# Kernel optimization log

Hardware: AMD Instinct MI355X
Metric: run time of the kernel (lower is better)

Reference implementation:

```python
import itertools
import jax, jax.numpy as jnp
import numpy as np

B, N, C, H = 4, 48, 16, 64
CIN = [48, 64, 128, 192]   # per-order MLP input dims after expand/reduce/concat/permute
COUT = 16

def _exclude_mask(n, cnt, dtype):
    # mask[i1..icnt] = 1 iff all object indices are pairwise distinct
    if cnt <= 1:
        return jnp.ones((n,), dtype=dtype)
    idx = [jnp.arange(n).reshape((1,) * d + (n,) + (1,) * (cnt - 1 - d)) for d in range(cnt)]
    m = jnp.ones((n,) * cnt, dtype=bool)
    for a in range(cnt):
        for b in range(a + 1, cnt):
            m = m & (idx[a] != idx[b])
    return m.astype(dtype)

def _reduce(x, dim):
    # x: [B] + [n]*dim + [C]; exists=max / forall=min over last object axis, exclude_self mask
    n = x.shape[1]
    m = _exclude_mask(n, dim, x.dtype)[..., None]  # [n]*dim + [1], broadcasts over B and C
    ex = jnp.max(x * m, axis=-2)
    fa = jnp.min(x * m + (1.0 - m), axis=-2)
    out = jnp.stack([ex, fa], axis=-1)  # interleave (exists, forall) per channel
    return out.reshape(out.shape[:-2] + (out.shape[-2] * 2,))

def _expand(x, dim, n):
    # insert a new object axis at position dim+1 and broadcast to n
    return jnp.broadcast_to(jnp.expand_dims(x, dim + 1), x.shape[:dim + 1] + (n,) + x.shape[dim + 1:])

def _permute(x, dim):
    # concat all permutations of the object axes along channels
    if dim <= 1:
        return x
    parts = [jnp.transpose(x, (0,) + p + (dim + 1,)) for p in itertools.permutations(range(1, dim + 1))]
    return jnp.concatenate(parts, axis=-1)

def _logic(x, W1, b1, W2, b2):
    # LogicInferenceLayer: Linear -> ReLU -> Linear -> Sigmoid on channel axis
    return jax.nn.sigmoid(jax.nn.relu(x @ W1 + b1) @ W2 + b2)

def setup_inputs() -> dict:
    key = jax.random.key(0)
    ks = jax.random.split(key, 24)
    inp = {
        'x0': jax.random.uniform(ks[0], (B, C), dtype=jnp.float32),
        'x1': jax.random.uniform(ks[1], (B, N, C), dtype=jnp.float32),
        'x2': jax.random.uniform(ks[2], (B, N, N, C), dtype=jnp.float32),
        'x3': jax.random.uniform(ks[3], (B, N, N, N, C), dtype=jnp.float32),
    }
    for o, cin in enumerate(CIN):
        inp[f'W1_{o}'] = jax.random.normal(ks[4 + 4 * o], (cin, H), dtype=jnp.float32) * 0.05
        inp[f'b1_{o}'] = jnp.zeros((H,), dtype=jnp.float32)
        inp[f'W2_{o}'] = jax.random.normal(ks[5 + 4 * o], (H, COUT), dtype=jnp.float32) * 0.05
        inp[f'b2_{o}'] = jnp.zeros((COUT,), dtype=jnp.float32)
    return inp

def reference(x0, x1, x2, x3,
              W1_0, b1_0, W2_0, b2_0,
              W1_1, b1_1, W2_1, b2_1,
              W1_2, b1_2, W2_2, b2_2,
              W1_3, b1_3, W2_3, b2_3):
    n = x1.shape[1]
    # order 0: [self, reduce(order1)]
    t0 = jnp.concatenate([x0, _reduce(x1, 1)], axis=-1)
    y0 = _logic(t0, W1_0, b1_0, W2_0, b2_0)
    # order 1: [expand(order0), self, reduce(order2)]
    t1 = jnp.concatenate([_expand(x0, 0, n), x1, _reduce(x2, 2)], axis=-1)
    y1 = _logic(t1, W1_1, b1_1, W2_1, b2_1)
    # order 2: [expand(order1), self, reduce(order3)], permute 2 object axes
    t2 = jnp.concatenate([_expand(x1, 1, n), x2, _reduce(x3, 3)], axis=-1)
    y2 = _logic(_permute(t2, 2), W1_2, b1_2, W2_2, b2_2)
    # order 3 (max order): [expand(order2), self], permute 3 object axes
    t3 = jnp.concatenate([_expand(x2, 2, n), x3], axis=-1)
    y3 = _logic(_permute(t3, 3), W1_3, b1_3, W2_3, b2_3)
    return (y0, y1, y2, y3)
```

## Files before the change

kernel.cpp:

```cpp
#include <hip/hip_runtime.h>
#include <hip/hip_bf16.h>


typedef __bf16 bf16x8 __attribute__((ext_vector_type(8)));
typedef unsigned short us8 __attribute__((ext_vector_type(8)));
typedef float f32x4 __attribute__((ext_vector_type(4)));

#define NPAIR 589824
#define NRED3 294912
#define NX3   7077888

__device__ __forceinline__ unsigned short f2bf(float f) {
    __hip_bfloat16 h = __float2bfloat16(f);
    return __builtin_bit_cast(unsigned short, h);
}
__device__ __forceinline__ unsigned int pk2(float a, float b) {
    return (unsigned int)f2bf(a) | ((unsigned int)f2bf(b) << 16);
}
__device__ __forceinline__ float bflo(unsigned int u) {
    return __builtin_bit_cast(float, u << 16);
}
__device__ __forceinline__ float bfhi(unsigned int u) {
    return __builtin_bit_cast(float, u & 0xffff0000u);
}
__device__ __forceinline__ float sigmoidf_(float z) {
    return 1.0f / (1.0f + __expf(-z));
}
__device__ __forceinline__ bf16x8 ld_bf8(const unsigned short* p) {
    return __builtin_bit_cast(bf16x8, *(const us8*)p);
}
__device__ __forceinline__ bf16x8 pack8(float4 a, float4 b) {
    us8 u;
    u[0] = f2bf(a.x); u[1] = f2bf(a.y); u[2] = f2bf(a.z); u[3] = f2bf(a.w);
    u[4] = f2bf(b.x); u[5] = f2bf(b.y); u[6] = f2bf(b.z); u[7] = f2bf(b.w);
    return __builtin_bit_cast(bf16x8, u);
}

__global__ __launch_bounds__(192) void perm3_kernel(
    const float* __restrict__ x3,
    unsigned short* __restrict__ X0, unsigned short* __restrict__ XA,
    unsigned short* __restrict__ XB)
{
    const int g = blockIdx.x;
    const int m2 = g % 48, t1 = g / 48, m1 = t1 % 48, b = t1 / 48;
    const int t = threadIdx.x;
    const int m3 = t >> 2, cq = (t & 3) * 4;
    const float4 v = *(const float4*)(x3 + (size_t)g * 768 + m3 * 16 + cq);
    const uint2 u = make_uint2(pk2(v.x, v.y), pk2(v.z, v.w));
    *(uint2*)(X0 + (size_t)g * 768 + m3 * 16 + cq) = u;
    *(uint2*)(XA + (((size_t)(b * 48 + m1) * 48 + m3) * 48 + m2) * 16 + cq) = u;
    *(uint2*)(XB + (((size_t)(b * 48 + m2) * 48 + m3) * 48 + m1) * 16 + cq) = u;
}

__global__ __launch_bounds__(256) void phaseA_kernel(
    const float* __restrict__ x2, const float* __restrict__ W1,
    const float* __restrict__ b1,
    float* __restrict__ wsA, unsigned short* __restrict__ wsB,
    unsigned short* __restrict__ wsC)
{
    __shared__ float xr[4][32];
    const int t = threadIdx.x;
    if (t < 128) {
        const int pr2 = t >> 5, c = t & 31;
        const int gg = blockIdx.x * 4 + pr2;
        const int bb = gg / 2304, pp2 = gg % 2304, P = pp2 / 48, Q = pp2 % 48;
        const float* base = x2 + (size_t)bb * 36864;
        xr[pr2][c] = (c < 16) ? base[(P * 48 + Q) * 16 + c]
                              : base[(Q * 48 + P) * 16 + (c - 16)];
    }
    __syncthreads();
    const int pr = t >> 6, h = t & 63;
    const int g = blockIdx.x * 4 + pr;
    float a = b1[h], bacc = 0.f, cacc = 0.f;
#pragma unroll
    for (int c = 0; c < 16; ++c) {
        const float xpq = xr[pr][c], xqp = xr[pr][16 + c];
        a    += xpq * W1[(  0 + c) * 64 + h] + xqp * W1[( 64 + c) * 64 + h];
        bacc += xpq * W1[( 32 + c) * 64 + h] + xqp * W1[( 96 + c) * 64 + h];
        cacc += xpq * W1[(128 + c) * 64 + h] + xqp * W1[(160 + c) * 64 + h];
    }
    const size_t o = (size_t)g * 64 + h;
    wsA[o] = a;
    wsB[o] = f2bf(bacc);
    wsC[o] = f2bf(cacc);
}

__global__ __launch_bounds__(192, 3) void y3_kernel(
    const unsigned short* __restrict__ X0,
    const unsigned short* __restrict__ XA,
    const unsigned short* __restrict__ XB,
    const float* __restrict__ W1, const float* __restrict__ W2,
    const float* __restrict__ b2,
    const float* __restrict__ wsA,
    const unsigned short* __restrict__ wsB,
    const unsigned short* __restrict__ wsC,
    float* __restrict__ out)
{
    __shared__ __align__(16) unsigned short w1t[64 * 104];
    const int t = threadIdx.x;
    const int w = t >> 6, lane = t & 63, lr = lane & 15, lg = lane >> 4;

#pragma unroll
    for (int p = 0; p < 16; ++p) {
        const int e = p * 192 + t;
        const int h = e & 63, kk = (e >> 6) * 2;
        const int r0 = 16 + ((kk >> 4) << 5) + (kk & 15);
        *(unsigned int*)(w1t + h * 104 + kk) =
            pk2(W1[r0 * 64 + h], W1[(r0 + 1) * 64 + h]);
    }
    __syncthreads();

    bf16x8 w1f[4][3];
#pragma unroll
    for (int n = 0; n < 4; ++n)
#pragma unroll
        for (int ks = 0; ks < 3; ++ks)
            w1f[n][ks] = ld_bf8(w1t + (16 * n + lr) * 104 + 32 * ks + 8 * lg);

    bf16x8 w2f[2];
#pragma unroll
    for (int m = 0; m < 2; ++m) {
        us8 u;
#pragma unroll
        for (int e = 0; e < 8; ++e) {
            const int ch = 16 * (e >> 1) + 4 * lg + 2 * (e & 1) + m;
            u[e] = f2bf(W2[ch * 16 + lr]);
        }
        w2f[m] = __builtin_bit_cast(bf16x8, u);
    }
    const float4 b2v = *(const float4*)(b2 + 4 * lg);
    const int row = 16 * w + lr;
    const int roff = row * 16 + 8 * (lg & 1);
    const bool hi = (lg >> 1) != 0;

    for (int it = 0; it < 4; ++it) {
        const int g = blockIdx.x * 4 + it;
        const int b = g / 2304, pp = g % 2304, i = pp / 48, j = pp % 48;
        const size_t blkIJ = ((size_t)(b * 48 + i) * 48 + j) * 768;
        const size_t blkJI = ((size_t)(b * 48 + j) * 48 + i) * 768;
        const unsigned short* p0 = (hi ? XA + blkIJ : X0 + blkIJ) + roff;
        const unsigned short* p1 = (hi ? XB + blkIJ : X0 + blkJI) + roff;
        const unsigned short* p2 = (hi ? XB + blkJI : XA + blkJI) + roff;
        const bf16x8 xf0 = ld_bf8(p0);
        const bf16x8 xf1 = ld_bf8(p1);
        const bf16x8 xf2 = ld_bf8(p2);

        f32x4 acc[4];
#pragma unroll
        for (int n = 0; n < 4; ++n) {
            acc[n] = f32x4{0.f, 0.f, 0.f, 0.f};
            acc[n] = __builtin_amdgcn_mfma_f32_16x16x32_bf16(w1f[n][0], xf0, acc[n], 0, 0, 0);
            acc[n] = __builtin_amdgcn_mfma_f32_16x16x32_bf16(w1f[n][1], xf1, acc[n], 0, 0, 0);
            acc[n] = __builtin_amdgcn_mfma_f32_16x16x32_bf16(w1f[n][2], xf2, acc[n], 0, 0, 0);
        }
        const size_t baseB = ((size_t)((b * 48 + i) * 48 + row)) * 64 + 4 * lg;
        const size_t baseC = ((size_t)((b * 48 + j) * 48 + row)) * 64 + 4 * lg;
        const size_t baseA = ((size_t)((b * 48 + i) * 48 + j)) * 64 + 4 * lg;
#pragma unroll
        for (int n = 0; n < 4; ++n) {
            const uint2 Bu = *(const uint2*)(wsB + baseB + 16 * n);
            const uint2 Cu = *(const uint2*)(wsC + baseC + 16 * n);
            const float4 Au = *(const float4*)(wsA + baseA + 16 * n);
            acc[n][0] = fmaxf(acc[n][0] + Au.x + bflo(Bu.x) + bflo(Cu.x), 0.f);
            acc[n][1] = fmaxf(acc[n][1] + Au.y + bfhi(Bu.x) + bfhi(Cu.x), 0.f);
            acc[n][2] = fmaxf(acc[n][2] + Au.z + bflo(Bu.y) + bflo(Cu.y), 0.f);
            acc[n][3] = fmaxf(acc[n][3] + Au.w + bfhi(Bu.y) + bfhi(Cu.y), 0.f);
        }
        bf16x8 hf[2];
#pragma unroll
        for (int m = 0; m < 2; ++m) {
            us8 u;
#pragma unroll
            for (int e = 0; e < 8; ++e)
                u[e] = f2bf(acc[e >> 1][2 * (e & 1) + m]);
            hf[m] = __builtin_bit_cast(bf16x8, u);
        }
        f32x4 o2 = {0.f, 0.f, 0.f, 0.f};
        o2 = __builtin_amdgcn_mfma_f32_16x16x32_bf16(w2f[0], hf[0], o2, 0, 0, 0);
        o2 = __builtin_amdgcn_mfma_f32_16x16x32_bf16(w2f[1], hf[1], o2, 0, 0, 0);
        float4 ov;
        ov.x = sigmoidf_(o2[0] + b2v.x);
        ov.y = sigmoidf_(o2[1] + b2v.y);
        ov.z = sigmoidf_(o2[2] + b2v.z);
        ov.w = sigmoidf_(o2[3] + b2v.w);
        *(float4*)(out + (size_t)g * 768 + row * 16 + 4 * lg) = ov;
    }
}

__global__ __launch_bounds__(192, 3) void y3_gather_kernel(
    const float* __restrict__ x3,
    const float* __restrict__ W1, const float* __restrict__ W2,
    const float* __restrict__ b2,
    const float* __restrict__ wsA,
    const unsigned short* __restrict__ wsB,
    const unsigned short* __restrict__ wsC,
    float* __restrict__ out)
{
    __shared__ __align__(16) unsigned short w1t[64 * 104];
    const int t = threadIdx.x;
    const int w = t >> 6, lane = t & 63, lr = lane & 15, lg = lane >> 4;
#pragma unroll
    for (int p = 0; p < 16; ++p) {
        const int e = p * 192 + t;
        const int h = e & 63, kk = (e >> 6) * 2;
        const int r0 = 16 + ((kk >> 4) << 5) + (kk & 15);
        *(unsigned int*)(w1t + h * 104 + kk) =
            pk2(W1[r0 * 64 + h], W1[(r0 + 1) * 64 + h]);
    }
    __syncthreads();
    bf16x8 w1f[4][3];
#pragma unroll
    for (int n = 0; n < 4; ++n)
#pragma unroll
        for (int ks = 0; ks < 3; ++ks)
            w1f[n][ks] = ld_bf8(w1t + (16 * n + lr) * 104 + 32 * ks + 8 * lg);
    bf16x8 w2f[2];
#pragma unroll
    for (int m = 0; m < 2; ++m) {
        us8 u;
#pragma unroll
        for (int e = 0; e < 8; ++e) {
            const int ch = 16 * (e >> 1) + 4 * lg + 2 * (e & 1) + m;
            u[e] = f2bf(W2[ch * 16 + lr]);
        }
        w2f[m] = __builtin_bit_cast(bf16x8, u);
    }
    const float4 b2v = *(const float4*)(b2 + 4 * lg);
    const int row = 16 * w + lr;
    const int c0 = 8 * (lg & 1);
    const bool hi = (lg >> 1) != 0;
    for (int it = 0; it < 4; ++it) {
        const int g = blockIdx.x * 4 + it;
        const int b = g / 2304, pp = g % 2304, i = pp / 48, j = pp % 48;
        const float* xb3 = x3 + (size_t)b * 1769472;
        const int sb0 = i * 36864 + j * 768 + row * 16;
        const int sb1 = i * 36864 + row * 768 + j * 16;
        const int sb2 = j * 36864 + i * 768 + row * 16;
        const int sb3 = row * 36864 + i * 768 + j * 16;
        const int sb4 = j * 36864 + row * 768 + i * 16;
        const int sb5 = row * 36864 + j * 768 + i * 16;
        const float* p0 = xb3 + (hi ? sb1 : sb0) + c0;
        const float* p1 = xb3 + (hi ? sb3 : sb2) + c0;
        const float* p2 = xb3 + (hi ? sb5 : sb4) + c0;
        const bf16x8 xf0 = pack8(*(const float4*)p0, *(const float4*)(p0 + 4));
        const bf16x8 xf1 = pack8(*(const float4*)p1, *(const float4*)(p1 + 4));
        const bf16x8 xf2 = pack8(*(const float4*)p2, *(const float4*)(p2 + 4));
        f32x4 acc[4];
#pragma unroll
        for (int n = 0; n < 4; ++n) {
            acc[n] = f32x4{0.f, 0.f, 0.f, 0.f};
            acc[n] = __builtin_amdgcn_mfma_f32_16x16x32_bf16(w1f[n][0], xf0, acc[n], 0, 0, 0);
            acc[n] = __builtin_amdgcn_mfma_f32_16x16x32_bf16(w1f[n][1], xf1, acc[n], 0, 0, 0);
            acc[n] = __builtin_amdgcn_mfma_f32_16x16x32_bf16(w1f[n][2], xf2, acc[n], 0, 0, 0);
        }
        const size_t baseB = ((size_t)((b * 48 + i) * 48 + row)) * 64 + 4 * lg;
        const size_t baseC = ((size_t)((b * 48 + j) * 48 + row)) * 64 + 4 * lg;
        const size_t baseA = ((size_t)((b * 48 + i) * 48 + j)) * 64 + 4 * lg;
#pragma unroll
        for (int n = 0; n < 4; ++n) {
            const uint2 Bu = *(const uint2*)(wsB + baseB + 16 * n);
            const uint2 Cu = *(const uint2*)(wsC + baseC + 16 * n);
            const float4 Au = *(const float4*)(wsA + baseA + 16 * n);
            acc[n][0] = fmaxf(acc[n][0] + Au.x + bflo(Bu.x) + bflo(Cu.x), 0.f);
            acc[n][1] = fmaxf(acc[n][1] + Au.y + bfhi(Bu.x) + bfhi(Cu.x), 0.f);
            acc[n][2] = fmaxf(acc[n][2] + Au.z + bflo(Bu.y) + bflo(Cu.y), 0.f);
            acc[n][3] = fmaxf(acc[n][3] + Au.w + bfhi(Bu.y) + bfhi(Cu.y), 0.f);
        }
        bf16x8 hf[2];
#pragma unroll
        for (int m = 0; m < 2; ++m) {
            us8 u;
#pragma unroll
            for (int e = 0; e < 8; ++e)
                u[e] = f2bf(acc[e >> 1][2 * (e & 1) + m]);
            hf[m] = __builtin_bit_cast(bf16x8, u);
        }
        f32x4 o2 = {0.f, 0.f, 0.f, 0.f};
        o2 = __builtin_amdgcn_mfma_f32_16x16x32_bf16(w2f[0], hf[0], o2, 0, 0, 0);
        o2 = __builtin_amdgcn_mfma_f32_16x16x32_bf16(w2f[1], hf[1], o2, 0, 0, 0);
        float4 ov;
        ov.x = sigmoidf_(o2[0] + b2v.x);
        ov.y = sigmoidf_(o2[1] + b2v.y);
        ov.z = sigmoidf_(o2[2] + b2v.z);
        ov.w = sigmoidf_(o2[3] + b2v.w);
        *(float4*)(out + (size_t)g * 768 + row * 16 + 4 * lg) = ov;
    }
}

__global__ __launch_bounds__(256) void red3_kernel(
    const float* __restrict__ x3, unsigned short* __restrict__ red3)
{
    const int slot = blockIdx.x * 256 + threadIdx.x;
    const int c = slot & 15;
    const int q = slot >> 4;
    const int j = q % 48, pi = q / 48, i = pi % 48;
    const float* p = x3 + (size_t)q * 768 + c;
    float ex = -__builtin_inff(), fa = __builtin_inff();
    const bool mij = (i != j);
#pragma unroll 8
    for (int k = 0; k < 48; ++k) {
        const bool m = mij & (k != i) & (k != j);
        const float v = p[k * 16];
        ex = fmaxf(ex, m ? v : 0.f);
        fa = fminf(fa, m ? v : 1.f);
    }
    *(unsigned int*)(red3 + (size_t)q * 32 + 2 * c) = pk2(ex, fa);
}

__global__ __launch_bounds__(192, 3) void y2_mlp_kernel(
    const float* __restrict__ x1, const float* __restrict__ x2,
    const float* __restrict__ W1, const float* __restrict__ b1,
    const float* __restrict__ W2, const float* __restrict__ b2,
    const unsigned short* __restrict__ red3, float* __restrict__ out)
{
    __shared__ __align__(16) unsigned short w1t[64 * 136];
    const int t = threadIdx.x;
    const int w = t >> 6, lane = t & 63, lr = lane & 15, lg = lane >> 4;

#pragma unroll
    for (int p = 0; p < 22; ++p) {
        const int e = p * 192 + t;
        if (e < 4096) {
            const int h = e & 63, k2 = e >> 6;
            *(unsigned int*)(w1t + h * 136 + 2 * k2) =
                pk2(W1[(2 * k2) * 64 + h], W1[(2 * k2 + 1) * 64 + h]);
        }
    }
    __syncthreads();

    bf16x8 w1f[4][4];
#pragma unroll
    for (int n = 0; n < 4; ++n)
#pragma unroll
        for (int ks = 0; ks < 4; ++ks)
            w1f[n][ks] = ld_bf8(w1t + (16 * n + lr) * 136 + 32 * ks + 8 * lg);

    bf16x8 w2f[2];
#pragma unroll
    for (int m = 0; m < 2; ++m) {
        us8 u;
#pragma unroll
        for (int e = 0; e < 8; ++e) {
            const int ch = 16 * (e >> 1) + 4 * lg + 2 * (e & 1) + m;
            u[e] = f2bf(W2[ch * 16 + lr]);
        }
        w2f[m] = __builtin_bit_cast(bf16x8, u);
    }
    float4 b1v[4];
#pragma unroll
    for (int n = 0; n < 4; ++n) b1v[n] = *(const float4*)(b1 + 16 * n + 4 * lg);
    const float4 b2v = *(const float4*)(b2 + 4 * lg);

    const int bq = blockIdx.x;
    const int b = bq / 48, i = bq % 48;
    const float* x2b = x2 + (size_t)b * 36864;
    const int row = 16 * w + lr;
    const int j = row;
    const int c0 = 8 * (lg & 1);
    const bool hi = (lg >> 1) != 0;

    const float* a0 = hi ? (x2b + (i * 48 + j) * 16 + c0) : (x1 + (b * 48 + i) * 16 + c0);
    const float* a2 = hi ? (x2b + (j * 48 + i) * 16 + c0) : (x1 + (b * 48 + j) * 16 + c0);
    const unsigned short* r1 = red3 + ((size_t)(b * 48 + i) * 48 + j) * 32 + (hi ? 16 : 0) + c0;
    const unsigned short* r3 = red3 + ((size_t)(b * 48 + j) * 48 + i) * 32 + (hi ? 16 : 0) + c0;

    const bf16x8 xf0 = pack8(*(const float4*)a0, *(const float4*)(a0 + 4));
    const bf16x8 xf1 = ld_bf8(r1);
    const bf16x8 xf2 = pack8(*(const float4*)a2, *(const float4*)(a2 + 4));
    const bf16x8 xf3 = ld_bf8(r3);

    f32x4 acc[4];
#pragma unroll
    for (int n = 0; n < 4; ++n) {
        acc[n] = f32x4{0.f, 0.f, 0.f, 0.f};
        acc[n] = __builtin_amdgcn_mfma_f32_16x16x32_bf16(w1f[n][0], xf0, acc[n], 0, 0, 0);
        acc[n] = __builtin_amdgcn_mfma_f32_16x16x32_bf16(w1f[n][1], xf1, acc[n], 0, 0, 0);
        acc[n] = __builtin_amdgcn_mfma_f32_16x16x32_bf16(w1f[n][2], xf2, acc[n], 0, 0, 0);
        acc[n] = __builtin_amdgcn_mfma_f32_16x16x32_bf16(w1f[n][3], xf3, acc[n], 0, 0, 0);
    }
#pragma unroll
    for (int n = 0; n < 4; ++n) {
        acc[n][0] = fmaxf(acc[n][0] + b1v[n].x, 0.f);
        acc[n][1] = fmaxf(acc[n][1] + b1v[n].y, 0.f);
        acc[n][2] = fmaxf(acc[n][2] + b1v[n].z, 0.f);
        acc[n][3] = fmaxf(acc[n][3] + b1v[n].w, 0.f);
    }
    bf16x8 hf[2];
#pragma unroll
    for (int m = 0; m < 2; ++m) {
        us8 u;
#pragma unroll
        for (int e = 0; e < 8; ++e)
            u[e] = f2bf(acc[e >> 1][2 * (e & 1) + m]);
        hf[m] = __builtin_bit_cast(bf16x8, u);
    }
    f32x4 o2 = {0.f, 0.f, 0.f, 0.f};
    o2 = __builtin_amdgcn_mfma_f32_16x16x32_bf16(w2f[0], hf[0], o2, 0, 0, 0);
    o2 = __builtin_amdgcn_mfma_f32_16x16x32_bf16(w2f[1], hf[1], o2, 0, 0, 0);
    float4 ov;
    ov.x = sigmoidf_(o2[0] + b2v.x);
    ov.y = sigmoidf_(o2[1] + b2v.y);
    ov.z = sigmoidf_(o2[2] + b2v.z);
    ov.w = sigmoidf_(o2[3] + b2v.w);
    *(float4*)(out + ((size_t)bq * 48 + row) * 16 + 4 * lg) = ov;
}

__global__ __launch_bounds__(192, 1) void y01_kernel(
    const float* __restrict__ x0, const float* __restrict__ x1,
    const float* __restrict__ x2,
    const float* __restrict__ W1_0, const float* __restrict__ b1_0,
    const float* __restrict__ W2_0, const float* __restrict__ b2_0,
    const float* __restrict__ W1_1, const float* __restrict__ b1_1,
    const float* __restrict__ W2_1, const float* __restrict__ b2_1,
    float* __restrict__ out)
{
    const int t = threadIdx.x;
    if (blockIdx.x < 4) {
        __shared__ __align__(16) unsigned short w1t[64 * 72];
        __shared__ __align__(16) unsigned short red2l[48 * 32];
        const int b = blockIdx.x;
#pragma unroll
        for (int p = 0; p < 11; ++p) {
            const int e = p * 192 + t;
            if (e < 2048) {
                const int h = e & 63, k2 = e >> 6;
                *(unsigned int*)(w1t + h * 72 + 2 * k2) =
                    pk2(W1_1[(2 * k2) * 64 + h], W1_1[(2 * k2 + 1) * 64 + h]);
            }
        }
        const float* x2b = x2 + (size_t)b * 36864;
#pragma unroll
        for (int s4 = 0; s4 < 4; ++s4) {
            const int s = t + 192 * s4;
            const int i = s >> 4, c = s & 15;
            const float* p = x2b + i * 768 + c;
            float ex = -__builtin_inff(), fa = __builtin_inff();
#pragma unroll 8
            for (int jj = 0; jj < 48; ++jj) {
                const bool m = (jj != i);
                const float v = p[jj * 16];
                ex = fmaxf(ex, m ? v : 0.f);
                fa = fminf(fa, m ? v : 1.f);
            }
            *(unsigned int*)(red2l + i * 32 + 2 * c) = pk2(ex, fa);
        }
        __syncthreads();

        const int w = t >> 6, lane = t & 63, lr = lane & 15, lg = lane >> 4;
        const int i = 16 * w + lr;
        const int rho = b * 48 + i;
        bf16x8 w1f[4][2];
#pragma unroll
        for (int n = 0; n < 4; ++n)
#pragma unroll
            for (int ks = 0; ks < 2; ++ks)
                w1f[n][ks] = ld_bf8(w1t + (16 * n + lr) * 72 + 32 * ks + 8 * lg);
        bf16x8 w2f[2];
#pragma unroll
        for (int m = 0; m < 2; ++m) {
            us8 u;
#pragma unroll
            for (int e = 0; e < 8; ++e) {
                const int ch = 16 * (e >> 1) + 4 * lg + 2 * (e & 1) + m;
                u[e] = f2bf(W2_1[ch * 16 + lr]);
            }
            w2f[m] = __builtin_bit_cast(bf16x8, u);
        }
        float4 b1v[4];
#pragma unroll
        for (int n = 0; n < 4; ++n) b1v[n] = *(const float4*)(b1_1 + 16 * n + 4 * lg);
        const float4 b2v = *(const float4*)(b2_1 + 4 * lg);

        const int c0 = 8 * (lg & 1);
        const float* a0 = (lg < 2) ? (x0 + b * 16 + c0) : (x1 + rho * 16 + c0);
        const bf16x8 xf0 = pack8(*(const float4*)a0, *(const float4*)(a0 + 4));
        const bf16x8 xf1 = ld_bf8(red2l + i * 32 + 8 * lg);

        f32x4 acc[4];
#pragma unroll
        for (int n = 0; n < 4; ++n) {
            acc[n] = f32x4{0.f, 0.f, 0.f, 0.f};
            acc[n] = __builtin_amdgcn_mfma_f32_16x16x32_bf16(w1f[n][0], xf0, acc[n], 0, 0, 0);
            acc[n] = __builtin_amdgcn_mfma_f32_16x16x32_bf16(w1f[n][1], xf1, acc[n], 0, 0, 0);
        }
#pragma unroll
        for (int n = 0; n < 4; ++n) {
            acc[n][0] = fmaxf(acc[n][0] + b1v[n].x, 0.f);
            acc[n][1] = fmaxf(acc[n][1] + b1v[n].y, 0.f);
            acc[n][2] = fmaxf(acc[n][2] + b1v[n].z, 0.f);
            acc[n][3] = fmaxf(acc[n][3] + b1v[n].w, 0.f);
        }
        bf16x8 hf[2];
#pragma unroll
        for (int m = 0; m < 2; ++m) {
            us8 u;
#pragma unroll
            for (int e = 0; e < 8; ++e)
                u[e] = f2bf(acc[e >> 1][2 * (e & 1) + m]);
            hf[m] = __builtin_bit_cast(bf16x8, u);
        }
        f32x4 o2 = {0.f, 0.f, 0.f, 0.f};
        o2 = __builtin_amdgcn_mfma_f32_16x16x32_bf16(w2f[0], hf[0], o2, 0, 0, 0);
        o2 = __builtin_amdgcn_mfma_f32_16x16x32_bf16(w2f[1], hf[1], o2, 0, 0, 0);
        float4 ov;
        ov.x = sigmoidf_(o2[0] + b2v.x);
        ov.y = sigmoidf_(o2[1] + b2v.y);
        ov.z = sigmoidf_(o2[2] + b2v.z);
        ov.w = sigmoidf_(o2[3] + b2v.w);
        *(float4*)(out + 64 + (size_t)rho * 16 + 4 * lg) = ov;
    } else {
        __shared__ float t0l[4][56];
        __shared__ float hl[4][72];
        if (t < 64) {
            const int b = t >> 4, c = t & 15;
            const float* p = x1 + b * 768 + c;
            float ex = -__builtin_inff(), fa = __builtin_inff();
#pragma unroll 8
            for (int n = 0; n < 48; ++n) {
                const float v = p[n * 16];
                ex = fmaxf(ex, v);
                fa = fminf(fa, v);
            }
            t0l[b][c] = x0[b * 16 + c];
            t0l[b][16 + 2 * c] = ex;
            t0l[b][17 + 2 * c] = fa;
        }
        __syncthreads();
        if (t < 64) {
            const int h = t;
            float ac0 = b1_0[h], ac1 = ac0, ac2 = ac0, ac3 = ac0;
#pragma unroll
            for (int c = 0; c < 48; ++c) {
                const float wv = W1_0[c * 64 + h];
                ac0 = fmaf(t0l[0][c], wv, ac0);
                ac1 = fmaf(t0l[1][c], wv, ac1);
                ac2 = fmaf(t0l[2][c], wv, ac2);
                ac3 = fmaf(t0l[3][c], wv, ac3);
            }
            hl[0][h] = fmaxf(ac0, 0.f);
            hl[1][h] = fmaxf(ac1, 0.f);
            hl[2][h] = fmaxf(ac2, 0.f);
            hl[3][h] = fmaxf(ac3, 0.f);
        }
        __syncthreads();
        if (t < 64) {
            const int b = t >> 4, o = t & 15;
            float a = b2_0[o];
#pragma unroll
            for (int h = 0; h < 64; ++h)
                a = fmaf(hl[b][h], W2_0[h * 16 + o], a);
            out[b * 16 + o] = sigmoidf_(a);
        }
    }
}

template <int NK>
__device__ __forceinline__ void mlp_head(
    const unsigned short* lds_in, const unsigned short* lds_w1t,
    const unsigned short* lds_w2t, const float* lds_b1, const float* lds_b2,
    unsigned short* lds_h, float* outp)
{
    constexpr int S = NK * 32 + 8;
    const int t = threadIdx.x;
    const int w = t >> 6, lr = t & 15, lg = (t >> 4) & 3;
    f32x4 acc0 = {0.f, 0.f, 0.f, 0.f};
    f32x4 acc1 = acc0, acc2 = acc0, acc3 = acc0;
    const unsigned short* pa = lds_in + (16 * w + lr) * S + lg * 8;
    const unsigned short* pb = lds_w1t + lr * S + lg * 8;
#pragma unroll
    for (int ks = 0; ks < NK; ++ks) {
        bf16x8 a = ld_bf8(pa + ks * 32);
        acc0 = __builtin_amdgcn_mfma_f32_16x16x32_bf16(a, ld_bf8(pb + 0 * 16 * S + ks * 32), acc0, 0, 0, 0);
        acc1 = __builtin_amdgcn_mfma_f32_16x16x32_bf16(a, ld_bf8(pb + 1 * 16 * S + ks * 32), acc1, 0, 0, 0);
        acc2 = __builtin_amdgcn_mfma_f32_16x16x32_bf16(a, ld_bf8(pb + 2 * 16 * S + ks * 32), acc2, 0, 0, 0);
        acc3 = __builtin_amdgcn_mfma_f32_16x16x32_bf16(a, ld_bf8(pb + 3 * 16 * S + ks * 32), acc3, 0, 0, 0);
    }
    const int hrow = 16 * w + lg * 4;
#pragma unroll
    for (int r = 0; r < 4; ++r) {
        lds_h[(hrow + r) * 72 +  0 + lr] = f2bf(fmaxf(acc0[r] + lds_b1[ 0 + lr], 0.f));
        lds_h[(hrow + r) * 72 + 16 + lr] = f2bf(fmaxf(acc1[r] + lds_b1[16 + lr], 0.f));
        lds_h[(hrow + r) * 72 + 32 + lr] = f2bf(fmaxf(acc2[r] + lds_b1[32 + lr], 0.f));
        lds_h[(hrow + r) * 72 + 48 + lr] = f2bf(fmaxf(acc3[r] + lds_b1[48 + lr], 0.f));
    }
    __syncthreads();
    f32x4 o = {0.f, 0.f, 0.f, 0.f};
#pragma unroll
    for (int ks = 0; ks < 2; ++ks) {
        bf16x8 a = ld_bf8(lds_h + (16 * w + lr) * 72 + ks * 32 + lg * 8);
        bf16x8 b = ld_bf8(lds_w2t + lr * 72 + ks * 32 + lg * 8);
        o = __builtin_amdgcn_mfma_f32_16x16x32_bf16(a, b, o, 0, 0, 0);
    }
    const float b2v = lds_b2[lr];
#pragma unroll
    for (int r = 0; r < 4; ++r)
        outp[(hrow + r) * 16 + lr] = sigmoidf_(o[r] + b2v);
}

__global__ __launch_bounds__(192) void y3_fallback_kernel(
    const float* __restrict__ x2, const float* __restrict__ x3,
    const float* __restrict__ W1, const float* __restrict__ b1,
    const float* __restrict__ W2, const float* __restrict__ b2,
    float* __restrict__ out)
{
    __shared__ __align__(16) unsigned short lds_in[48 * 200];
    __shared__ __align__(16) unsigned short lds_w1t[64 * 200];
    __shared__ __align__(16) unsigned short lds_w2t[16 * 72];
    __shared__ __align__(16) unsigned short lds_h[48 * 72];
    __shared__ float lds_b1[64];
    __shared__ float lds_b2[16];
    const int t = threadIdx.x;
#pragma unroll 4
    for (int p = 0; p < 32; ++p) {
        int e = p * 192 + t;
        int h = e & 63, c2 = e >> 6;
        *(unsigned int*)(lds_w1t + h * 200 + 2 * c2) =
            pk2(W1[(2 * c2) * 64 + h], W1[(2 * c2 + 1) * 64 + h]);
    }
    for (int p = 0; p < 3; ++p) {
        int e = p * 192 + t;
        if (e < 512) {
            int n = e & 15, k2 = e >> 4;
            *(unsigned int*)(lds_w2t + n * 72 + 2 * k2) =
                pk2(W2[(2 * k2) * 16 + n], W2[(2 * k2 + 1) * 16 + n]);
        }
    }
    if (t < 64) lds_b1[t] = b1[t];
    if (t < 16) lds_b2[t] = b2[t];
    const int k = t >> 2, c4 = (t & 3) * 4;
#define STAGE3(PTR, BASE, KSTR, CH) do {                                       \
        const float4 v = *(const float4*)((PTR) + (BASE) + k * (KSTR) + c4);   \
        *(uint2*)(lds_in + k * 200 + (CH) + c4) =                              \
            make_uint2(pk2(v.x, v.y), pk2(v.z, v.w));                          \
    } while (0)
    for (int it = 0; it < 9; ++it) {
        const int g = blockIdx.x * 9 + it;
        const int b = g / 2304, rg = g % 2304, i = rg / 48, j = rg % 48;
        const float* xb2 = x2 + b * 36864;
        const float* xb3 = x3 + b * 1769472;
        __syncthreads();
        STAGE3(xb2, i * 768 + j * 16, 0,       0);
        STAGE3(xb3, i * 36864 + j * 768, 16,   16);
        STAGE3(xb2, i * 768, 16,               32);
        STAGE3(xb3, i * 36864 + j * 16, 768,   48);
        STAGE3(xb2, j * 768 + i * 16, 0,       64);
        STAGE3(xb3, j * 36864 + i * 768, 16,   80);
        STAGE3(xb2, i * 16, 768,               96);
        STAGE3(xb3, i * 768 + j * 16, 36864,   112);
        STAGE3(xb2, j * 768, 16,               128);
        STAGE3(xb3, j * 36864 + i * 16, 768,   144);
        STAGE3(xb2, j * 16, 768,               160);
        STAGE3(xb3, j * 768 + i * 16, 36864,   176);
        __syncthreads();
        mlp_head<6>(lds_in, lds_w1t, lds_w2t, lds_b1, lds_b2, lds_h,
                    out + (size_t)g * 768);
    }
#undef STAGE3
}

__global__ __launch_bounds__(192) void y2_kernel(
    const float* __restrict__ x1, const float* __restrict__ x2,
    const float* __restrict__ x3,
    const float* __restrict__ W1, const float* __restrict__ b1,
    const float* __restrict__ W2, const float* __restrict__ b2,
    float* __restrict__ out)
{
    __shared__ __align__(16) unsigned short lds_in[48 * 136];
    __shared__ __align__(16) unsigned short lds_w1t[64 * 136];
    __shared__ __align__(16) unsigned short lds_w2t[16 * 72];
    __shared__ __align__(16) unsigned short lds_h[48 * 72];
    __shared__ float lds_b1[64];
    __shared__ float lds_b2[16];
    const int t = threadIdx.x;
    const int b = blockIdx.x / 48, i = blockIdx.x % 48;
#pragma unroll 2
    for (int p = 0; p < 22; ++p) {
        int e = p * 192 + t;
        if (e < 4096) {
            int h = e & 63, c2 = e >> 6;
            *(unsigned int*)(lds_w1t + h * 136 + 2 * c2) =
                pk2(W1[(2 * c2) * 64 + h], W1[(2 * c2 + 1) * 64 + h]);
        }
    }
    for (int p = 0; p < 3; ++p) {
        int e = p * 192 + t;
        if (e < 512) {
            int n = e & 15, k2 = e >> 4;
            *(unsigned int*)(lds_w2t + n * 72 + 2 * k2) =
                pk2(W2[(2 * k2) * 16 + n], W2[(2 * k2 + 1) * 16 + n]);
        }
    }
    if (t < 64) lds_b1[t] = b1[t];
    if (t < 16) lds_b2[t] = b2[t];
    const int j = t >> 2, c4 = (t & 3) * 4;
    const float* xb2 = x2 + b * 36864;
#define STAGE2(PTR, BASE, JSTR, CH) do {                                       \
        const float4 v = *(const float4*)((PTR) + (BASE) + j * (JSTR) + c4);   \
        *(uint2*)(lds_in + j * 136 + (CH) + c4) =                              \
            make_uint2(pk2(v.x, v.y), pk2(v.z, v.w));                          \
    } while (0)
    STAGE2(x1, b * 768 + i * 16, 0,  0);
    STAGE2(xb2, i * 768, 16,         16);
    STAGE2(x1, b * 768, 16,          64);
    STAGE2(xb2, i * 16, 768,         80);
#undef STAGE2
    {
        const float* pa = x3 + b * 1769472 + (i * 48 + j) * 768 + c4;
        const float* pb = x3 + b * 1769472 + (j * 48 + i) * 768 + c4;
        float exa[4], faa[4], exb[4], fab[4];
#pragma unroll
        for (int u = 0; u < 4; ++u) {
            exa[u] = -__builtin_inff(); faa[u] = __builtin_inff();
            exb[u] = -__builtin_inff(); fab[u] = __builtin_inff();
        }
        for (int kk = 0; kk < 48; ++kk) {
            const bool m = (i != j) & (i != kk) & (j != kk);
            const float4 va = *(const float4*)(pa + kk * 16);
            const float4 vb = *(const float4*)(pb + kk * 16);
            const float av[4] = {va.x, va.y, va.z, va.w};
            const float bv[4] = {vb.x, vb.y, vb.z, vb.w};
#pragma unroll
            for (int u = 0; u < 4; ++u) {
                exa[u] = fmaxf(exa[u], m ? av[u] : 0.f);
                faa[u] = fminf(faa[u], m ? av[u] : 1.f);
                exb[u] = fmaxf(exb[u], m ? bv[u] : 0.f);
                fab[u] = fminf(fab[u], m ? bv[u] : 1.f);
            }
        }
#pragma unroll
        for (int u = 0; u < 4; ++u) {
            const int c = c4 + u;
            *(unsigned int*)(lds_in + j * 136 + 32 + 2 * c) = pk2(exa[u], faa[u]);
            *(unsigned int*)(lds_in + j * 136 + 96 + 2 * c) = pk2(exb[u], fab[u]);
        }
    }
    __syncthreads();
    mlp_head<4>(lds_in, lds_w1t, lds_w2t, lds_b1, lds_b2, lds_h,
                out + (size_t)blockIdx.x * 768);
}

extern "C" void kernel_launch(void* const* d_in, const int* in_sizes, int n_in,
                              void* d_out, int out_size, void* d_ws, size_t ws_size,
                              hipStream_t stream) {
    (void)in_sizes; (void)n_in; (void)out_size;
    const float* x0 = (const float*)d_in[0];
    const float* x1 = (const float*)d_in[1];
    const float* x2 = (const float*)d_in[2];
    const float* x3 = (const float*)d_in[3];
    const float* W1_0 = (const float*)d_in[4];
    const float* b1_0 = (const float*)d_in[5];
    const float* W2_0 = (const float*)d_in[6];
    const float* b2_0 = (const float*)d_in[7];
    const float* W1_1 = (const float*)d_in[8];
    const float* b1_1 = (const float*)d_in[9];
    const float* W2_1 = (const float*)d_in[10];
    const float* b2_1 = (const float*)d_in[11];
    const float* W1_2 = (const float*)d_in[12];
    const float* b1_2 = (const float*)d_in[13];
    const float* W2_2 = (const float*)d_in[14];
    const float* b2_2 = (const float*)d_in[15];
    const float* W1_3 = (const float*)d_in[16];
    const float* b1_3 = (const float*)d_in[17];
    const float* W2_3 = (const float*)d_in[18];
    const float* b2_3 = (const float*)d_in[19];
    float* out = (float*)d_out;

    const size_t ws_mid  = (size_t)8 * NPAIR + (size_t)2 * NRED3;
    const size_t ws_full = ws_mid + (size_t)6 * NX3;
    if (ws_size >= ws_mid) {
        float* wsA = (float*)d_ws;
        unsigned short* wsB = (unsigned short*)d_ws + 2 * NPAIR;
        unsigned short* wsC = wsB + NPAIR;
        unsigned short* red3 = (unsigned short*)d_ws + 4 * NPAIR;
        phaseA_kernel<<<2304, 256, 0, stream>>>(x2, W1_3, b1_3, wsA, wsB, wsC);
        if (ws_size >= ws_full) {
            unsigned short* X0 = red3 + NRED3;
            unsigned short* XA = X0 + NX3;
            unsigned short* XB = XA + NX3;
            perm3_kernel<<<9216, 192, 0, stream>>>(x3, X0, XA, XB);
            y3_kernel<<<2304, 192, 0, stream>>>(X0, XA, XB, W1_3, W2_3, b2_3,
                                                wsA, wsB, wsC, out + 150592);
        } else {
            y3_gather_kernel<<<2304, 192, 0, stream>>>(x3, W1_3, W2_3, b2_3,
                                                       wsA, wsB, wsC, out + 150592);
        }
        red3_kernel<<<576, 256, 0, stream>>>(x3, red3);
        y2_mlp_kernel<<<192, 192, 0, stream>>>(x1, x2, W1_2, b1_2, W2_2, b2_2,
                                               red3, out + 3136);
    } else {
        y3_fallback_kernel<<<1024, 192, 0, stream>>>(x2, x3, W1_3, b1_3, W2_3, b2_3,
                                                     out + 150592);
        y2_kernel<<<192, 192, 0, stream>>>(x1, x2, x3, W1_2, b1_2, W2_2, b2_2,
                                           out + 3136);
    }
    y01_kernel<<<5, 192, 0, stream>>>(x0, x1, x2, W1_0, b1_0, W2_0, b2_0,
                                      W1_1, b1_1, W2_1, b2_1, out);
}
```

Baseline: 207.1 us.

## Fuse order-3 reduction into permute kernel and pipeline y3 tiles over j

```diff
diff --git a/kernel.cpp b/kernel.cpp
--- a/kernel.cpp
+++ b/kernel.cpp
@@ -39,17 +39,33 @@
 __global__ __launch_bounds__(192) void perm3_kernel(
     const float* __restrict__ x3,
     unsigned short* __restrict__ X0, unsigned short* __restrict__ XA,
-    unsigned short* __restrict__ XB)
-{
+    unsigned short* __restrict__ XB, unsigned short* __restrict__ red3)
+{
+    __shared__ float rowf[768];
     const int g = blockIdx.x;
     const int m2 = g % 48, t1 = g / 48, m1 = t1 % 48, b = t1 / 48;
     const int t = threadIdx.x;
     const int m3 = t >> 2, cq = (t & 3) * 4;
     const float4 v = *(const float4*)(x3 + (size_t)g * 768 + m3 * 16 + cq);
+    *(float4*)(rowf + m3 * 16 + cq) = v;
     const uint2 u = make_uint2(pk2(v.x, v.y), pk2(v.z, v.w));
     *(uint2*)(X0 + (size_t)g * 768 + m3 * 16 + cq) = u;
     *(uint2*)(XA + (((size_t)(b * 48 + m1) * 48 + m3) * 48 + m2) * 16 + cq) = u;
     *(uint2*)(XB + (((size_t)(b * 48 + m2) * 48 + m3) * 48 + m1) * 16 + cq) = u;
+    __syncthreads();
+    if (t < 16) {
+        const int c = t;
+        float ex = -__builtin_inff(), fa = __builtin_inff();
+        const bool mij = (m1 != m2);
+#pragma unroll 8
+        for (int k = 0; k < 48; ++k) {
+            const bool m = mij & (k != m1) & (k != m2);
+            const float vv = rowf[k * 16 + c];
+            ex = fmaxf(ex, m ? vv : 0.f);
+            fa = fminf(fa, m ? vv : 1.f);
+        }
+        *(unsigned int*)(red3 + (size_t)g * 32 + 2 * c) = pk2(ex, fa);
+    }
 }
 
 __global__ __launch_bounds__(256) void phaseA_kernel(
@@ -84,6 +100,8 @@
     wsB[o] = f2bf(bacc);
     wsC[o] = f2bf(cacc);
 }
+
+#define Y3_TILES 8
 
 __global__ __launch_bounds__(192, 3) void y3_kernel(
     const unsigned short* __restrict__ X0,
@@ -133,38 +151,61 @@
     const int roff = row * 16 + 8 * (lg & 1);
     const bool hi = (lg >> 1) != 0;
 
-    for (int it = 0; it < 4; ++it) {
-        const int g = blockIdx.x * 4 + it;
-        const int b = g / 2304, pp = g % 2304, i = pp / 48, j = pp % 48;
-        const size_t blkIJ = ((size_t)(b * 48 + i) * 48 + j) * 768;
-        const size_t blkJI = ((size_t)(b * 48 + j) * 48 + i) * 768;
-        const unsigned short* p0 = (hi ? XA + blkIJ : X0 + blkIJ) + roff;
-        const unsigned short* p1 = (hi ? XB + blkIJ : X0 + blkJI) + roff;
-        const unsigned short* p2 = (hi ? XB + blkJI : XA + blkJI) + roff;
-        const bf16x8 xf0 = ld_bf8(p0);
-        const bf16x8 xf1 = ld_bf8(p1);
-        const bf16x8 xf2 = ld_bf8(p2);
-
+    const int g0 = blockIdx.x * Y3_TILES;
+    const int b = g0 / 2304, pp = g0 % 2304, i = pp / 48, j0 = pp % 48;
+
+    const size_t baseB = ((size_t)((b * 48 + i) * 48 + row)) * 64 + 4 * lg;
+    uint2 Bu[4];
+#pragma unroll
+    for (int n = 0; n < 4; ++n) Bu[n] = *(const uint2*)(wsB + baseB + 16 * n);
+
+    const size_t rowIJ = ((size_t)(b * 48 + i) * 48) * 768;
+
+    bf16x8 xc0, xc1, xc2;
+    uint2 Cu[4];
+    {
+        const size_t bIJ = rowIJ + (size_t)j0 * 768;
+        const size_t bJI = ((size_t)(b * 48 + j0) * 48 + i) * 768;
+        xc0 = ld_bf8((hi ? XA + bIJ : X0 + bIJ) + roff);
+        xc1 = ld_bf8((hi ? XB + bIJ : X0 + bJI) + roff);
+        xc2 = ld_bf8((hi ? XB + bJI : XA + bJI) + roff);
+        const size_t baseC = ((size_t)((b * 48 + j0) * 48 + row)) * 64 + 4 * lg;
+#pragma unroll
+        for (int n = 0; n < 4; ++n) Cu[n] = *(const uint2*)(wsC + baseC + 16 * n);
+    }
+
+#pragma unroll
+    for (int it = 0; it < Y3_TILES; ++it) {
+        const int j = j0 + it;
+        bf16x8 xn0, xn1, xn2;
+        uint2 Cn[4];
+        if (it < Y3_TILES - 1) {
+            const int jn = j + 1;
+            const size_t bIJ = rowIJ + (size_t)jn * 768;
+            const size_t bJI = ((size_t)(b * 48 + jn) * 48 + i) * 768;
+            xn0 = ld_bf8((hi ? XA + bIJ : X0 + bIJ) + roff);
+            xn1 = ld_bf8((hi ? XB + bIJ : X0 + bJI) + roff);
+            xn2 = ld_bf8((hi ? XB + bJI : XA + bJI) + roff);
+            const size_t baseC = ((size_t)((b * 48 + jn) * 48 + row)) * 64 + 4 * lg;
+#pragma unroll
+            for (int n = 0; n < 4; ++n) Cn[n] = *(const uint2*)(wsC + baseC + 16 * n);
+        }
         f32x4 acc[4];
 #pragma unroll
         for (int n = 0; n < 4; ++n) {
             acc[n] = f32x4{0.f, 0.f, 0.f, 0.f};
-            acc[n] = __builtin_amdgcn_mfma_f32_16x16x32_bf16(w1f[n][0], xf0, acc[n], 0, 0, 0);
-            acc[n] = __builtin_amdgcn_mfma_f32_16x16x32_bf16(w1f[n][1], xf1, acc[n], 0, 0, 0);
-            acc[n] = __builtin_amdgcn_mfma_f32_16x16x32_bf16(w1f[n][2], xf2, acc[n], 0, 0, 0);
-        }
-        const size_t baseB = ((size_t)((b * 48 + i) * 48 + row)) * 64 + 4 * lg;
-        const size_t baseC = ((size_t)((b * 48 + j) * 48 + row)) * 64 + 4 * lg;
+            acc[n] = __builtin_amdgcn_mfma_f32_16x16x32_bf16(w1f[n][0], xc0, acc[n], 0, 0, 0);
+            acc[n] = __builtin_amdgcn_mfma_f32_16x16x32_bf16(w1f[n][1], xc1, acc[n], 0, 0, 0);
+            acc[n] = __builtin_amdgcn_mfma_f32_16x16x32_bf16(w1f[n][2], xc2, acc[n], 0, 0, 0);
+        }
         const size_t baseA = ((size_t)((b * 48 + i) * 48 + j)) * 64 + 4 * lg;
 #pragma unroll
         for (int n = 0; n < 4; ++n) {
-            const uint2 Bu = *(const uint2*)(wsB + baseB + 16 * n);
-            const uint2 Cu = *(const uint2*)(wsC + baseC + 16 * n);
             const float4 Au = *(const float4*)(wsA + baseA + 16 * n);
-            acc[n][0] = fmaxf(acc[n][0] + Au.x + bflo(Bu.x) + bflo(Cu.x), 0.f);
-            acc[n][1] = fmaxf(acc[n][1] + Au.y + bfhi(Bu.x) + bfhi(Cu.x), 0.f);
-            acc[n][2] = fmaxf(acc[n][2] + Au.z + bflo(Bu.y) + bflo(Cu.y), 0.f);
-            acc[n][3] = fmaxf(acc[n][3] + Au.w + bfhi(Bu.y) + bfhi(Cu.y), 0.f);
+            acc[n][0] = fmaxf(acc[n][0] + Au.x + bflo(Bu[n].x) + bflo(Cu[n].x), 0.f);
+            acc[n][1] = fmaxf(acc[n][1] + Au.y + bfhi(Bu[n].x) + bfhi(Cu[n].x), 0.f);
+            acc[n][2] = fmaxf(acc[n][2] + Au.z + bflo(Bu[n].y) + bflo(Cu[n].y), 0.f);
+            acc[n][3] = fmaxf(acc[n][3] + Au.w + bfhi(Bu[n].y) + bfhi(Cu[n].y), 0.f);
         }
         bf16x8 hf[2];
 #pragma unroll
@@ -183,7 +224,12 @@
         ov.y = sigmoidf_(o2[1] + b2v.y);
         ov.z = sigmoidf_(o2[2] + b2v.z);
         ov.w = sigmoidf_(o2[3] + b2v.w);
-        *(float4*)(out + (size_t)g * 768 + row * 16 + 4 * lg) = ov;
+        *(float4*)(out + (size_t)(g0 + it) * 768 + row * 16 + 4 * lg) = ov;
+        if (it < Y3_TILES - 1) {
+            xc0 = xn0; xc1 = xn1; xc2 = xn2;
+#pragma unroll
+            for (int n = 0; n < 4; ++n) Cu[n] = Cn[n];
+        }
     }
 }
 
@@ -777,14 +823,14 @@
             unsigned short* X0 = red3 + NRED3;
             unsigned short* XA = X0 + NX3;
             unsigned short* XB = XA + NX3;
-            perm3_kernel<<<9216, 192, 0, stream>>>(x3, X0, XA, XB);
-            y3_kernel<<<2304, 192, 0, stream>>>(X0, XA, XB, W1_3, W2_3, b2_3,
-                                                wsA, wsB, wsC, out + 150592);
+            perm3_kernel<<<9216, 192, 0, stream>>>(x3, X0, XA, XB, red3);
+            y3_kernel<<<9216 / Y3_TILES, 192, 0, stream>>>(
+                X0, XA, XB, W1_3, W2_3, b2_3, wsA, wsB, wsC, out + 150592);
         } else {
             y3_gather_kernel<<<2304, 192, 0, stream>>>(x3, W1_3, W2_3, b2_3,
                                                        wsA, wsB, wsC, out + 150592);
-        }
-        red3_kernel<<<576, 256, 0, stream>>>(x3, red3);
+            red3_kernel<<<576, 256, 0, stream>>>(x3, red3);
+        }
         y2_mlp_kernel<<<192, 192, 0, stream>>>(x1, x2, W1_2, b1_2, W2_2, b2_2,
                                                red3, out + 3136);
     } else {
```

Measured after the change: 184.0 us. -11.2%, faster.
